# Optimization experiments

Hardware: AMD Instinct MI355X
Metric: run time of the kernel (lower is better)

Reference implementation:

```python
import jax, jax.numpy as jnp
import numpy as np

N = 50000      # nodes
E2 = 400000    # undirected edges
E = 2 * E2     # directed edges (each undirected edge in both directions)
DIN = 512      # input feature dim
DH = 128       # MLP hidden
C = 8          # num classes / BP channels


def setup_inputs() -> dict:
    key = jax.random.key(0)
    ks = jax.random.split(key, 9)
    x = jax.random.normal(ks[0], (N, DIN), jnp.float32)
    src0 = jax.random.randint(ks[1], (E2,), 0, N)
    dst0 = jax.random.randint(ks[2], (E2,), 0, N)
    # symmetric directed edge list: row 0 = source j, row 1 = target i
    edge_index = jnp.stack([jnp.concatenate([src0, dst0]),
                            jnp.concatenate([dst0, src0])])
    w0 = jax.random.uniform(ks[3], (E2,), jnp.float32, 0.5, 1.5)
    edge_weight = jnp.concatenate([w0, w0])  # reverse edge shares weight
    # edge_rv[e] = index of the reverse of edge e
    edge_rv = jnp.concatenate([jnp.arange(E2) + E2, jnp.arange(E2)])
    W1 = jax.random.normal(ks[4], (DIN, DH), jnp.float32) * 0.05
    b1 = jnp.zeros((DH,), jnp.float32)
    W2 = jax.random.normal(ks[5], (DH, C), jnp.float32) * 0.05
    b2 = jnp.zeros((C,), jnp.float32)
    param = jax.random.normal(ks[6], (C, C), jnp.float32) * 0.1
    return {"x": x, "edge_index": edge_index, "edge_weight": edge_weight,
            "edge_rv": edge_rv, "W1": W1, "b1": b1, "W2": W2, "b2": b2,
            "param": param, "K": 5}


def log_normalize(log_x):
    return log_x - jax.nn.logsumexp(log_x, axis=-1, keepdims=True)


def reference(x, edge_index, edge_weight, edge_rv, W1, b1, W2, b2, param, K):
    # MLP transform + LogSoftmax -> initial log-beliefs [N, C]
    h = jax.nn.relu(x @ W1 + b1)
    log_b0 = jax.nn.log_softmax(h @ W2 + b2, axis=-1)

    # learn_H=True: logH = logsigmoid(param + param^T), [C, C]
    logH = jax.nn.log_sigmoid(param + param.T)
    src, dst = edge_index[0], edge_index[1]
    # per-edge coupling matrix [E, C, C]
    logC = edge_weight[:, None, None] * logH[None, :, :]

    log_b = log_b0
    log_msg = None
    for _ in range(K):
        x_j = log_b[src]                       # gather source beliefs [E, C]
        if log_msg is not None:
            x_j = x_j - log_msg[edge_rv]       # remove reverse message
        # tropical-semiring matvec in log domain: logsumexp over source channel
        log_msg = log_normalize(jax.nn.logsumexp(x_j[:, :, None] + logC, axis=1))
        agg = jax.ops.segment_sum(log_msg, dst, num_segments=N)  # scatter-add
        log_b = log_normalize(log_b0 + agg)
    return log_b
```

## Files before the change

kernel.cpp:

```cpp
#include <hip/hip_runtime.h>
#include <hip/hip_bf16.h>
#include <hip/hip_fp16.h>
#include <math.h>

#define NN 50000
#define EE 800000
#define E2K 400000
#define DINK 512
#define DHK 128
#define CK 8
#define KIT 5
#define NBLKS 196
#define NPB 32
#define CAP 1024

typedef __attribute__((ext_vector_type(8))) short short8;
typedef __attribute__((ext_vector_type(4))) float f32x4;

__device__ __forceinline__ unsigned short f2bf(float f) {
    union { float f; unsigned int u; } v;
    v.f = f;
    unsigned int u = v.u;
    unsigned int r = (u + 0x7FFFu + ((u >> 16) & 1u)) >> 16;
    return (unsigned short)r;
}
__device__ __forceinline__ float bfu2f(unsigned int lo16) {
    union { unsigned int u; float f; } v;
    v.u = lo16 << 16;
    return v.f;
}

__global__ __launch_bounds__(256) void prep_kernel(
    const float* __restrict__ W1, const float* __restrict__ param,
    unsigned short* __restrict__ W1t, float* __restrict__ logH) {
    if (blockIdx.x < 256) {
        int idx = blockIdx.x * 256 + threadIdx.x;
        int n = idx >> 9;
        int k = idx & 511;
        W1t[idx] = f2bf(W1[(size_t)k * DHK + n]);
    } else if (threadIdx.x < 64) {
        int t = threadIdx.x;
        int i = t >> 3, j = t & 7;
        float z = param[i * 8 + j] + param[j * 8 + i];
        logH[t] = fminf(z, 0.0f) - log1pf(expf(-fabsf(z)));
    }
}

__global__ __launch_bounds__(256) void mlp_mfma_kernel(
    const float* __restrict__ x, const unsigned short* __restrict__ W1t,
    const float* __restrict__ b1, const float* __restrict__ W2,
    const float* __restrict__ b2, float* __restrict__ logb0) {
    __shared__ unsigned short hs[64 * 136];
    __shared__ float W2s[128 * 8];
    __shared__ float b1s[128];
    __shared__ float b2s[8];

    const int tid = threadIdx.x;
    const int wave = tid >> 6;
    const int lane = tid & 63;
    const int q = lane >> 4;
    const int lm = lane & 15;
    const int wm = wave >> 1, wn = wave & 1;
    const int n0 = blockIdx.x * 64;

    if (tid < 128) b1s[tid] = b1[tid];
    if (tid < 8) b2s[tid] = b2[tid];
    {
        int i = tid * 4;
        *(float4*)&W2s[i] = *(const float4*)&W2[i];
    }
    __syncthreads();

    const float* xptr[2];
#pragma unroll
    for (int mt = 0; mt < 2; ++mt) {
        int r = n0 + wm * 32 + mt * 16 + lm;
        if (r > NN - 1) r = NN - 1;
        xptr[mt] = x + (size_t)r * DINK + q * 8;
    }
    const unsigned short* bptr[4];
#pragma unroll
    for (int nt = 0; nt < 4; ++nt) {
        int c = wn * 64 + nt * 16 + lm;
        bptr[nt] = W1t + (size_t)c * DINK + q * 8;
    }

    f32x4 acc[2][4];
#pragma unroll
    for (int mt = 0; mt < 2; ++mt)
#pragma unroll
        for (int nt = 0; nt < 4; ++nt) acc[mt][nt] = (f32x4){0.f, 0.f, 0.f, 0.f};

    float4 ar[2][2];
    short8 bc[4];
#pragma unroll
    for (int mt = 0; mt < 2; ++mt) {
        ar[mt][0] = *(const float4*)(xptr[mt]);
        ar[mt][1] = *(const float4*)(xptr[mt] + 4);
    }
#pragma unroll
    for (int nt = 0; nt < 4; ++nt) bc[nt] = *(const short8*)(bptr[nt]);

#pragma unroll
    for (int k0 = 32; k0 <= DINK; k0 += 32) {
        float4 ar2[2][2];
        short8 b2f[4];
        if (k0 < DINK) {
#pragma unroll
            for (int mt = 0; mt < 2; ++mt) {
                ar2[mt][0] = *(const float4*)(xptr[mt] + k0);
                ar2[mt][1] = *(const float4*)(xptr[mt] + k0 + 4);
            }
#pragma unroll
            for (int nt = 0; nt < 4; ++nt)
                b2f[nt] = *(const short8*)(bptr[nt] + k0);
        }
        short8 af[2];
#pragma unroll
        for (int mt = 0; mt < 2; ++mt) {
            union { short8 s; __hip_bfloat162 h[4]; } cv;
            cv.h[0] = __float22bfloat162_rn(make_float2(ar[mt][0].x, ar[mt][0].y));
            cv.h[1] = __float22bfloat162_rn(make_float2(ar[mt][0].z, ar[mt][0].w));
            cv.h[2] = __float22bfloat162_rn(make_float2(ar[mt][1].x, ar[mt][1].y));
            cv.h[3] = __float22bfloat162_rn(make_float2(ar[mt][1].z, ar[mt][1].w));
            af[mt] = cv.s;
        }
#pragma unroll
        for (int mt = 0; mt < 2; ++mt)
#pragma unroll
            for (int nt = 0; nt < 4; ++nt)
                acc[mt][nt] = __builtin_amdgcn_mfma_f32_16x16x32_bf16(
                    af[mt], bc[nt], acc[mt][nt], 0, 0, 0);
        if (k0 < DINK) {
#pragma unroll
            for (int mt = 0; mt < 2; ++mt) {
                ar[mt][0] = ar2[mt][0];
                ar[mt][1] = ar2[mt][1];
            }
#pragma unroll
            for (int nt = 0; nt < 4; ++nt) bc[nt] = b2f[nt];
        }
    }

#pragma unroll
    for (int nt = 0; nt < 4; ++nt) {
        int j = wn * 64 + nt * 16 + lm;
        float bj = b1s[j];
#pragma unroll
        for (int mt = 0; mt < 2; ++mt) {
            int rbase = wm * 32 + mt * 16 + q * 4;
#pragma unroll
            for (int r = 0; r < 4; ++r) {
                float h = fmaxf(acc[mt][nt][r] + bj, 0.0f);
                hs[(rbase + r) * 136 + j] = f2bf(h);
            }
        }
    }
    __syncthreads();

    int row = tid >> 2;
    int qh = tid & 3;
    const unsigned short* hp = &hs[row * 136 + qh * 32];
    float p[8] = {0.f, 0.f, 0.f, 0.f, 0.f, 0.f, 0.f, 0.f};
#pragma unroll
    for (int ch = 0; ch < 4; ++ch) {
        uint4 c4 = *(const uint4*)(hp + ch * 8);
        unsigned int uu[4] = {c4.x, c4.y, c4.z, c4.w};
#pragma unroll
        for (int p2 = 0; p2 < 4; ++p2) {
            float h0 = bfu2f(uu[p2] & 0xFFFFu);
            float h1 = bfu2f(uu[p2] >> 16);
            int j = qh * 32 + ch * 8 + p2 * 2;
            const float* w0 = &W2s[j * 8];
            const float* w1 = &W2s[(j + 1) * 8];
#pragma unroll
            for (int c = 0; c < 8; ++c) p[c] = fmaf(h0, w0[c], p[c]);
#pragma unroll
            for (int c = 0; c < 8; ++c) p[c] = fmaf(h1, w1[c], p[c]);
        }
    }
#pragma unroll
    for (int c = 0; c < 8; ++c) p[c] += __shfl_xor(p[c], 1, 64);
#pragma unroll
    for (int c = 0; c < 8; ++c) p[c] += __shfl_xor(p[c], 2, 64);
    int grow = n0 + row;
    if (qh == 0 && grow < NN) {
        float v[8];
        float mx = -1e30f;
#pragma unroll
        for (int c = 0; c < 8; ++c) {
            v[c] = p[c] + b2s[c];
            mx = fmaxf(mx, v[c]);
        }
        float s = 0.0f;
#pragma unroll
        for (int c = 0; c < 8; ++c) s += expf(v[c] - mx);
        float ln = mx + logf(s);
        float4* p0 = (float4*)&logb0[(size_t)grow * 8];
        p0[0] = make_float4(v[0] - ln, v[1] - ln, v[2] - ln, v[3] - ln);
        p0[1] = make_float4(v[4] - ln, v[5] - ln, v[6] - ln, v[7] - ln);
    }
}


__global__ __launch_bounds__(256) void deg_pair_kernel(const int* __restrict__ ei,
                                                       int* __restrict__ cnt) {
    int e = blockIdx.x * 256 + threadIdx.x;
    if (e >= E2K) return;
    int s = ei[e];
    int d = ei[EE + e];
    atomicAdd(&cnt[d], 1);
    atomicAdd(&cnt[s], 1);
}

__global__ __launch_bounds__(256) void scan_partial_kernel(
    const int* __restrict__ cnt, int* __restrict__ partial) {
    __shared__ int sd[256];
    int t = threadIdx.x;
    int i = blockIdx.x * 256 + t;
    sd[t] = (i < NN) ? cnt[i] : 0;
    __syncthreads();
#pragma unroll
    for (int s = 128; s > 0; s >>= 1) {
        if (t < s) sd[t] += sd[t + s];
        __syncthreads();
    }
    if (t == 0) partial[blockIdx.x] = sd[0];
}

__global__ __launch_bounds__(256) void scan_tops_kernel(
    const int* __restrict__ partial, int* __restrict__ tops) {
    __shared__ int sd[256];
    int t = threadIdx.x;
    sd[t] = (t < NBLKS) ? partial[t] : 0;
    __syncthreads();
#pragma unroll
    for (int s = 1; s < 256; s <<= 1) {
        int a = sd[t];
        int b = (t >= s) ? sd[t - s] : 0;
        __syncthreads();
        sd[t] = a + b;
        __syncthreads();
    }
    if (t < NBLKS) tops[t] = (t > 0) ? sd[t - 1] : 0;
}

__global__ __launch_bounds__(256) void scan_write_kernel(
    const int* __restrict__ cnt, const int* __restrict__ tops,
    int* __restrict__ off) {
    __shared__ int sd[256];
    int t = threadIdx.x;
    int i = blockIdx.x * 256 + t;
    int v = (i < NN) ? cnt[i] : 0;
    sd[t] = v;
    __syncthreads();
#pragma unroll
    for (int s = 1; s < 256; s <<= 1) {
        int a = sd[t];
        int b = (t >= s) ? sd[t - s] : 0;
        __syncthreads();
        sd[t] = a + b;
        __syncthreads();
    }
    if (i < NN) off[i] = tops[blockIdx.x] + sd[t] - v;
    if (i == NN - 1) off[NN] = EE;
}

__global__ __launch_bounds__(256) void pos_pair_kernel(
    const int* __restrict__ ei, const float* __restrict__ ew,
    const int* __restrict__ off, int* __restrict__ cnt,
    int2* __restrict__ perm_sw, int2* __restrict__ perm_dr) {
    int e = blockIdx.x * 256 + threadIdx.x;
    if (e >= E2K) return;
    int s = ei[e];
    int d = ei[EE + e];
    int wbits = __float_as_int(ew[e]);
    int pA = off[d] + atomicAdd(&cnt[d], 1);
    int pB = off[s] + atomicAdd(&cnt[s], 1);
    int2 v;
    v.x = s; v.y = wbits; perm_sw[pA] = v;
    v.x = d;              perm_sw[pB] = v;
    v.x = d; v.y = pB;    perm_dr[pA] = v;
    v.x = s; v.y = pA;    perm_dr[pB] = v;
}

__global__ __launch_bounds__(256) void bp_iter_kernel(
    const float* __restrict__ logb0, const int* __restrict__ off,
    const int2* __restrict__ perm_sw, const int2* __restrict__ perm_dr,
    const float* __restrict__ logH, const uint4* __restrict__ msg_prev,
    uint4* __restrict__ msg_next, const float* __restrict__ bel_prev,
    float* __restrict__ bel_next, float* __restrict__ out,
    int first, int last) {
    __shared__ _Float16 smg[CAP * 8];
    __shared__ float lH[64];
    const int t = threadIdx.x;
    if (t < 64) lH[t] = logH[t];

    const int n0 = blockIdx.x * NPB;
    const int nend = (n0 + NPB < NN) ? (n0 + NPB) : NN;
    const int jb0 = off[n0];
    const int jb1 = off[nend];
    const int nl = t >> 3;
    const int c = t & 7;
    const int n = n0 + nl;

    float a = 0.0f;
    int jn0 = 0, jn1 = 0;
    if (n < nend) {
        jn0 = off[n];
        jn1 = off[n + 1];
        a = logb0[(size_t)n * 8 + c];
    }
    __syncthreads();

    for (int cb = jb0; cb < jb1; cb += CAP) {
        int ce = (cb + CAP < jb1) ? (cb + CAP) : jb1;
        for (int j = cb + t; j < ce; j += 256) {
            int2 sw = perm_sw[j];
            float w = __int_as_float(sw.y);
            const float4* pb = (const float4*)&bel_prev[(size_t)sw.x * 8];
            float4 v0 = pb[0], v1 = pb[1];
            float xj[8];
            xj[0] = v0.x; xj[1] = v0.y; xj[2] = v0.z; xj[3] = v0.w;
            xj[4] = v1.x; xj[5] = v1.y; xj[6] = v1.z; xj[7] = v1.w;
            if (!first) {
                int rvp = perm_dr[j].y;
                union { uint4 u; _Float16 h[8]; } mv;
                mv.u = msg_prev[rvp];
#pragma unroll
                for (int k = 0; k < 8; ++k) xj[k] -= (float)mv.h[k];
            }
            float M = xj[0];
#pragma unroll
            for (int k = 1; k < 8; ++k) M = fmaxf(M, xj[k]);
#pragma unroll
            for (int k = 0; k < 8; ++k) xj[k] -= M;
            float mg[8];
#pragma unroll
            for (int c2 = 0; c2 < 8; ++c2) {
                float ssum = 0.0f;
#pragma unroll
                for (int c1 = 0; c1 < 8; ++c1)
                    ssum += __expf(fmaf(w, lH[c1 * 8 + c2], xj[c1]));
                mg[c2] = __logf(ssum);
            }
            float mm = mg[0];
#pragma unroll
            for (int k = 1; k < 8; ++k) mm = fmaxf(mm, mg[k]);
            float se = 0.0f;
#pragma unroll
            for (int k = 0; k < 8; ++k) se += __expf(mg[k] - mm);
            float ln = mm + __logf(se);
            union { uint4 u; _Float16 h[8]; } ov;
#pragma unroll
            for (int k = 0; k < 8; ++k) ov.h[k] = (_Float16)(mg[k] - ln);
            *(uint4*)&smg[(j - cb) * 8] = ov.u;
            if (!last) msg_next[j] = ov.u;
        }
        __syncthreads();
        int lo = (jn0 > cb) ? jn0 : cb;
        int hi = (jn1 < ce) ? jn1 : ce;
        for (int j = lo; j < hi; ++j) a += (float)smg[(j - cb) * 8 + c];
        __syncthreads();
    }

    float mx = a;
#pragma unroll
    for (int s = 1; s < 8; s <<= 1) mx = fmaxf(mx, __shfl_xor(mx, s, 8));
    float sum = __expf(a - mx);
#pragma unroll
    for (int s = 1; s < 8; s <<= 1) sum += __shfl_xor(sum, s, 8);
    float v = a - (mx + __logf(sum));
    if (n < nend) {
        if (last) out[(size_t)n * 8 + c] = v;
        else bel_next[(size_t)n * 8 + c] = v;
    }
}

extern "C" void kernel_launch(void* const* d_in, const int* in_sizes, int n_in,
                              void* d_out, int out_size, void* d_ws, size_t ws_size,
                              hipStream_t stream) {
    const float* x = (const float*)d_in[0];
    const int* ei = (const int*)d_in[1];
    const float* ew = (const float*)d_in[2];
    const float* W1 = (const float*)d_in[4];
    const float* b1 = (const float*)d_in[5];
    const float* W2 = (const float*)d_in[6];
    const float* b2 = (const float*)d_in[7];
    const float* param = (const float*)d_in[8];
    float* out = (float*)d_out;

    float* wsf = (float*)d_ws;
    float* logH = wsf;
    float* logb0 = logH + 64;
    uint4* msgA = (uint4*)(logb0 + (size_t)NN * 8);
    uint4* msgB = msgA + EE;
    int* off = (int*)(msgB + EE);
    int2* perm_sw = (int2*)(off + 50004);
    int2* perm_dr = perm_sw + EE;
    unsigned short* W1t = (unsigned short*)(perm_dr + EE);
    float* belA = (float*)(W1t + 65536);
    float* belB = belA + (size_t)NN * 8;
    int* cnt = (int*)msgA;
    int* partial = cnt + NN;
    int* tops = partial + NBLKS;

    prep_kernel<<<257, 256, 0, stream>>>(W1, param, W1t, logH);
    mlp_mfma_kernel<<<(NN + 63) / 64, 256, 0, stream>>>(x, W1t, b1, W2, b2,
                                                        logb0);

    const int E2B = (E2K + 255) / 256;

    hipMemsetAsync(cnt, 0, (size_t)NN * sizeof(int), stream);
    deg_pair_kernel<<<E2B, 256, 0, stream>>>(ei, cnt);
    scan_partial_kernel<<<NBLKS, 256, 0, stream>>>(cnt, partial);
    scan_tops_kernel<<<1, 256, 0, stream>>>(partial, tops);
    scan_write_kernel<<<NBLKS, 256, 0, stream>>>(cnt, tops, off);
    hipMemsetAsync(cnt, 0, (size_t)NN * sizeof(int), stream);
    pos_pair_kernel<<<E2B, 256, 0, stream>>>(ei, ew, off, cnt, perm_sw, perm_dr);

    const int NB = (NN + NPB - 1) / NPB;
    uint4* msgs[2] = {msgA, msgB};
    float* bels[2] = {belA, belB};
    const float* bprev = logb0;
    for (int it = 0; it < KIT; ++it) {
        bp_iter_kernel<<<NB, 256, 0, stream>>>(
            logb0, off, perm_sw, perm_dr, logH,
            msgs[(it + 1) & 1] , msgs[it & 1] ,
            bprev, bels[it & 1], out,
            it == 0 ? 1 : 0, it == KIT - 1 ? 1 : 0);
        bprev = bels[it & 1];
    }
}
```

Baseline: 466.6 us.

## Split BP iteration into edge-parallel message and node aggregation kernels; enlarge MLP tile

Each fused BP iteration, which computed messages into LDS chunks per 32-node block and then aggregated them, is replaced by two kernels. An edge-parallel msg_kernel handles two edges per thread and always writes messages to global memory. A node-parallel agg_kernel then sums each node's incoming messages from global memory. The reverse-edge table shrinks from int2 to int, which cuts index traffic. The MLP kernel also processes 128 rows per block instead of 64, giving more register accumulators per wave and a 2-way rather than 4-way W2 reduction. In exchange there are extra launches, an added global write and read of messages on the last iteration, and higher register pressure in the MLP kernel.

```diff
diff --git a/kernel.cpp b/kernel.cpp
--- a/kernel.cpp
+++ b/kernel.cpp
@@ -11,8 +11,6 @@
 #define CK 8
 #define KIT 5
 #define NBLKS 196
-#define NPB 32
-#define CAP 1024
 
 typedef __attribute__((ext_vector_type(8))) short short8;
 typedef __attribute__((ext_vector_type(4))) float f32x4;
@@ -50,7 +48,7 @@
     const float* __restrict__ x, const unsigned short* __restrict__ W1t,
     const float* __restrict__ b1, const float* __restrict__ W2,
     const float* __restrict__ b2, float* __restrict__ logb0) {
-    __shared__ unsigned short hs[64 * 136];
+    __shared__ unsigned short hs[128 * 136];
     __shared__ float W2s[128 * 8];
     __shared__ float b1s[128];
     __shared__ float b2s[8];
@@ -61,7 +59,7 @@
     const int q = lane >> 4;
     const int lm = lane & 15;
     const int wm = wave >> 1, wn = wave & 1;
-    const int n0 = blockIdx.x * 64;
+    const int n0 = blockIdx.x * 128;
 
     if (tid < 128) b1s[tid] = b1[tid];
     if (tid < 8) b2s[tid] = b2[tid];
@@ -71,10 +69,10 @@
     }
     __syncthreads();
 
-    const float* xptr[2];
-#pragma unroll
-    for (int mt = 0; mt < 2; ++mt) {
-        int r = n0 + wm * 32 + mt * 16 + lm;
+    const float* xptr[4];
+#pragma unroll
+    for (int mt = 0; mt < 4; ++mt) {
+        int r = n0 + wm * 64 + mt * 16 + lm;
         if (r > NN - 1) r = NN - 1;
         xptr[mt] = x + (size_t)r * DINK + q * 8;
     }
@@ -85,16 +83,16 @@
         bptr[nt] = W1t + (size_t)c * DINK + q * 8;
     }
 
-    f32x4 acc[2][4];
-#pragma unroll
-    for (int mt = 0; mt < 2; ++mt)
+    f32x4 acc[4][4];
+#pragma unroll
+    for (int mt = 0; mt < 4; ++mt)
 #pragma unroll
         for (int nt = 0; nt < 4; ++nt) acc[mt][nt] = (f32x4){0.f, 0.f, 0.f, 0.f};
 
-    float4 ar[2][2];
+    float4 ar[4][2];
     short8 bc[4];
 #pragma unroll
-    for (int mt = 0; mt < 2; ++mt) {
+    for (int mt = 0; mt < 4; ++mt) {
         ar[mt][0] = *(const float4*)(xptr[mt]);
         ar[mt][1] = *(const float4*)(xptr[mt] + 4);
     }
@@ -103,11 +101,11 @@
 
 #pragma unroll
     for (int k0 = 32; k0 <= DINK; k0 += 32) {
-        float4 ar2[2][2];
+        float4 ar2[4][2];
         short8 b2f[4];
         if (k0 < DINK) {
 #pragma unroll
-            for (int mt = 0; mt < 2; ++mt) {
+            for (int mt = 0; mt < 4; ++mt) {
                 ar2[mt][0] = *(const float4*)(xptr[mt] + k0);
                 ar2[mt][1] = *(const float4*)(xptr[mt] + k0 + 4);
             }
@@ -115,9 +113,9 @@
             for (int nt = 0; nt < 4; ++nt)
                 b2f[nt] = *(const short8*)(bptr[nt] + k0);
         }
-        short8 af[2];
-#pragma unroll
-        for (int mt = 0; mt < 2; ++mt) {
+        short8 af[4];
+#pragma unroll
+        for (int mt = 0; mt < 4; ++mt) {
             union { short8 s; __hip_bfloat162 h[4]; } cv;
             cv.h[0] = __float22bfloat162_rn(make_float2(ar[mt][0].x, ar[mt][0].y));
             cv.h[1] = __float22bfloat162_rn(make_float2(ar[mt][0].z, ar[mt][0].w));
@@ -126,14 +124,14 @@
             af[mt] = cv.s;
         }
 #pragma unroll
-        for (int mt = 0; mt < 2; ++mt)
+        for (int mt = 0; mt < 4; ++mt)
 #pragma unroll
             for (int nt = 0; nt < 4; ++nt)
                 acc[mt][nt] = __builtin_amdgcn_mfma_f32_16x16x32_bf16(
                     af[mt], bc[nt], acc[mt][nt], 0, 0, 0);
         if (k0 < DINK) {
 #pragma unroll
-            for (int mt = 0; mt < 2; ++mt) {
+            for (int mt = 0; mt < 4; ++mt) {
                 ar[mt][0] = ar2[mt][0];
                 ar[mt][1] = ar2[mt][1];
             }
@@ -147,8 +145,8 @@
         int j = wn * 64 + nt * 16 + lm;
         float bj = b1s[j];
 #pragma unroll
-        for (int mt = 0; mt < 2; ++mt) {
-            int rbase = wm * 32 + mt * 16 + q * 4;
+        for (int mt = 0; mt < 4; ++mt) {
+            int rbase = wm * 64 + mt * 16 + q * 4;
 #pragma unroll
             for (int r = 0; r < 4; ++r) {
                 float h = fmaxf(acc[mt][nt][r] + bj, 0.0f);
@@ -158,19 +156,19 @@
     }
     __syncthreads();
 
-    int row = tid >> 2;
-    int qh = tid & 3;
-    const unsigned short* hp = &hs[row * 136 + qh * 32];
+    int row = tid >> 1;
+    int half = tid & 1;
+    const unsigned short* hp = &hs[row * 136 + half * 64];
     float p[8] = {0.f, 0.f, 0.f, 0.f, 0.f, 0.f, 0.f, 0.f};
 #pragma unroll
-    for (int ch = 0; ch < 4; ++ch) {
+    for (int ch = 0; ch < 8; ++ch) {
         uint4 c4 = *(const uint4*)(hp + ch * 8);
         unsigned int uu[4] = {c4.x, c4.y, c4.z, c4.w};
 #pragma unroll
         for (int p2 = 0; p2 < 4; ++p2) {
             float h0 = bfu2f(uu[p2] & 0xFFFFu);
             float h1 = bfu2f(uu[p2] >> 16);
-            int j = qh * 32 + ch * 8 + p2 * 2;
+            int j = half * 64 + ch * 8 + p2 * 2;
             const float* w0 = &W2s[j * 8];
             const float* w1 = &W2s[(j + 1) * 8];
 #pragma unroll
@@ -181,10 +179,8 @@
     }
 #pragma unroll
     for (int c = 0; c < 8; ++c) p[c] += __shfl_xor(p[c], 1, 64);
-#pragma unroll
-    for (int c = 0; c < 8; ++c) p[c] += __shfl_xor(p[c], 2, 64);
     int grow = n0 + row;
-    if (qh == 0 && grow < NN) {
+    if (half == 0 && grow < NN) {
         float v[8];
         float mx = -1e30f;
 #pragma unroll
@@ -269,7 +265,7 @@
 __global__ __launch_bounds__(256) void pos_pair_kernel(
     const int* __restrict__ ei, const float* __restrict__ ew,
     const int* __restrict__ off, int* __restrict__ cnt,
-    int2* __restrict__ perm_sw, int2* __restrict__ perm_dr) {
+    int2* __restrict__ perm_sw, int* __restrict__ rvp) {
     int e = blockIdx.x * 256 + threadIdx.x;
     if (e >= E2K) return;
     int s = ei[e];
@@ -280,90 +276,103 @@
     int2 v;
     v.x = s; v.y = wbits; perm_sw[pA] = v;
     v.x = d;              perm_sw[pB] = v;
-    v.x = d; v.y = pB;    perm_dr[pA] = v;
-    v.x = s; v.y = pA;    perm_dr[pB] = v;
-}
-
-__global__ __launch_bounds__(256) void bp_iter_kernel(
-    const float* __restrict__ logb0, const int* __restrict__ off,
-    const int2* __restrict__ perm_sw, const int2* __restrict__ perm_dr,
+    rvp[pA] = pB;
+    rvp[pB] = pA;
+}
+
+__global__ __launch_bounds__(256) void msg_kernel(
+    const int2* __restrict__ perm_sw, const int* __restrict__ rvp,
     const float* __restrict__ logH, const uint4* __restrict__ msg_prev,
-    uint4* __restrict__ msg_next, const float* __restrict__ bel_prev,
-    float* __restrict__ bel_next, float* __restrict__ out,
-    int first, int last) {
-    __shared__ _Float16 smg[CAP * 8];
+    const float* __restrict__ bel_prev, uint4* __restrict__ msg_next,
+    int first) {
     __shared__ float lH[64];
     const int t = threadIdx.x;
     if (t < 64) lH[t] = logH[t];
-
-    const int n0 = blockIdx.x * NPB;
-    const int nend = (n0 + NPB < NN) ? (n0 + NPB) : NN;
-    const int jb0 = off[n0];
-    const int jb1 = off[nend];
-    const int nl = t >> 3;
+    __syncthreads();
+
+    const int base = blockIdx.x * 512 + t;
+    int jj[2];
+    int2 sw[2];
+#pragma unroll
+    for (int e = 0; e < 2; ++e) {
+        int j = base + e * 256;
+        jj[e] = j;
+        int jc = (j < EE) ? j : (EE - 1);
+        sw[e] = perm_sw[jc];
+    }
+    float4 ba[2], bb[2];
+#pragma unroll
+    for (int e = 0; e < 2; ++e) {
+        const float4* pb = (const float4*)&bel_prev[(size_t)sw[e].x * 8];
+        ba[e] = pb[0];
+        bb[e] = pb[1];
+    }
+    uint4 mp[2];
+    if (!first) {
+        int rv[2];
+#pragma unroll
+        for (int e = 0; e < 2; ++e) {
+            int j = jj[e];
+            int jc = (j < EE) ? j : (EE - 1);
+            rv[e] = rvp[jc];
+        }
+#pragma unroll
+        for (int e = 0; e < 2; ++e) mp[e] = msg_prev[rv[e]];
+    }
+
+#pragma unroll
+    for (int e = 0; e < 2; ++e) {
+        float w = __int_as_float(sw[e].y);
+        float xj[8];
+        xj[0] = ba[e].x; xj[1] = ba[e].y; xj[2] = ba[e].z; xj[3] = ba[e].w;
+        xj[4] = bb[e].x; xj[5] = bb[e].y; xj[6] = bb[e].z; xj[7] = bb[e].w;
+        if (!first) {
+            union { uint4 u; _Float16 h[8]; } cv;
+            cv.u = mp[e];
+#pragma unroll
+            for (int k = 0; k < 8; ++k) xj[k] -= (float)cv.h[k];
+        }
+        float M = xj[0];
+#pragma unroll
+        for (int k = 1; k < 8; ++k) M = fmaxf(M, xj[k]);
+#pragma unroll
+        for (int k = 0; k < 8; ++k) xj[k] -= M;
+        float mg[8];
+#pragma unroll
+        for (int c2 = 0; c2 < 8; ++c2) {
+            float ssum = 0.0f;
+#pragma unroll
+            for (int c1 = 0; c1 < 8; ++c1)
+                ssum += __expf(fmaf(w, lH[c1 * 8 + c2], xj[c1]));
+            mg[c2] = __logf(ssum);
+        }
+        float mm = mg[0];
+#pragma unroll
+        for (int k = 1; k < 8; ++k) mm = fmaxf(mm, mg[k]);
+        float se = 0.0f;
+#pragma unroll
+        for (int k = 0; k < 8; ++k) se += __expf(mg[k] - mm);
+        float ln = mm + __logf(se);
+        union { uint4 u; _Float16 h[8]; } ov;
+#pragma unroll
+        for (int k = 0; k < 8; ++k) ov.h[k] = (_Float16)(mg[k] - ln);
+        if (jj[e] < EE) msg_next[jj[e]] = ov.u;
+    }
+}
+
+__global__ __launch_bounds__(256) void agg_kernel(
+    const float* __restrict__ logb0, const int* __restrict__ off,
+    const uint4* __restrict__ msg, float* __restrict__ bel_next,
+    float* __restrict__ out, int last) {
+    const int t = threadIdx.x;
+    const int n = blockIdx.x * 32 + (t >> 3);
     const int c = t & 7;
-    const int n = n0 + nl;
-
-    float a = 0.0f;
-    int jn0 = 0, jn1 = 0;
-    if (n < nend) {
-        jn0 = off[n];
-        jn1 = off[n + 1];
-        a = logb0[(size_t)n * 8 + c];
-    }
-    __syncthreads();
-
-    for (int cb = jb0; cb < jb1; cb += CAP) {
-        int ce = (cb + CAP < jb1) ? (cb + CAP) : jb1;
-        for (int j = cb + t; j < ce; j += 256) {
-            int2 sw = perm_sw[j];
-            float w = __int_as_float(sw.y);
-            const float4* pb = (const float4*)&bel_prev[(size_t)sw.x * 8];
-            float4 v0 = pb[0], v1 = pb[1];
-            float xj[8];
-            xj[0] = v0.x; xj[1] = v0.y; xj[2] = v0.z; xj[3] = v0.w;
-            xj[4] = v1.x; xj[5] = v1.y; xj[6] = v1.z; xj[7] = v1.w;
-            if (!first) {
-                int rvp = perm_dr[j].y;
-                union { uint4 u; _Float16 h[8]; } mv;
-                mv.u = msg_prev[rvp];
-#pragma unroll
-                for (int k = 0; k < 8; ++k) xj[k] -= (float)mv.h[k];
-            }
-            float M = xj[0];
-#pragma unroll
-            for (int k = 1; k < 8; ++k) M = fmaxf(M, xj[k]);
-#pragma unroll
-            for (int k = 0; k < 8; ++k) xj[k] -= M;
-            float mg[8];
-#pragma unroll
-            for (int c2 = 0; c2 < 8; ++c2) {
-                float ssum = 0.0f;
-#pragma unroll
-                for (int c1 = 0; c1 < 8; ++c1)
-                    ssum += __expf(fmaf(w, lH[c1 * 8 + c2], xj[c1]));
-                mg[c2] = __logf(ssum);
-            }
-            float mm = mg[0];
-#pragma unroll
-            for (int k = 1; k < 8; ++k) mm = fmaxf(mm, mg[k]);
-            float se = 0.0f;
-#pragma unroll
-            for (int k = 0; k < 8; ++k) se += __expf(mg[k] - mm);
-            float ln = mm + __logf(se);
-            union { uint4 u; _Float16 h[8]; } ov;
-#pragma unroll
-            for (int k = 0; k < 8; ++k) ov.h[k] = (_Float16)(mg[k] - ln);
-            *(uint4*)&smg[(j - cb) * 8] = ov.u;
-            if (!last) msg_next[j] = ov.u;
-        }
-        __syncthreads();
-        int lo = (jn0 > cb) ? jn0 : cb;
-        int hi = (jn1 < ce) ? jn1 : ce;
-        for (int j = lo; j < hi; ++j) a += (float)smg[(j - cb) * 8 + c];
-        __syncthreads();
-    }
-
+    if (n >= NN) return;
+    float a = logb0[(size_t)n * 8 + c];
+    const int j0 = off[n];
+    const int j1 = off[n + 1];
+    const _Float16* mh = (const _Float16*)msg;
+    for (int j = j0; j < j1; ++j) a += (float)mh[(size_t)j * 8 + c];
     float mx = a;
 #pragma unroll
     for (int s = 1; s < 8; s <<= 1) mx = fmaxf(mx, __shfl_xor(mx, s, 8));
@@ -371,10 +380,8 @@
 #pragma unroll
     for (int s = 1; s < 8; s <<= 1) sum += __shfl_xor(sum, s, 8);
     float v = a - (mx + __logf(sum));
-    if (n < nend) {
-        if (last) out[(size_t)n * 8 + c] = v;
-        else bel_next[(size_t)n * 8 + c] = v;
-    }
+    if (last) out[(size_t)n * 8 + c] = v;
+    else bel_next[(size_t)n * 8 + c] = v;
 }
 
 extern "C" void kernel_launch(void* const* d_in, const int* in_sizes, int n_in,
@@ -397,8 +404,8 @@
     uint4* msgB = msgA + EE;
     int* off = (int*)(msgB + EE);
     int2* perm_sw = (int2*)(off + 50004);
-    int2* perm_dr = perm_sw + EE;
-    unsigned short* W1t = (unsigned short*)(perm_dr + EE);
+    int* rvp = (int*)(perm_sw + EE);
+    unsigned short* W1t = (unsigned short*)(rvp + EE);
     float* belA = (float*)(W1t + 65536);
     float* belB = belA + (size_t)NN * 8;
     int* cnt = (int*)msgA;
@@ -406,8 +413,8 @@
     int* tops = partial + NBLKS;
 
     prep_kernel<<<257, 256, 0, stream>>>(W1, param, W1t, logH);
-    mlp_mfma_kernel<<<(NN + 63) / 64, 256, 0, stream>>>(x, W1t, b1, W2, b2,
-                                                        logb0);
+    mlp_mfma_kernel<<<(NN + 127) / 128, 256, 0, stream>>>(x, W1t, b1, W2, b2,
+                                                          logb0);
 
     const int E2B = (E2K + 255) / 256;
 
@@ -417,18 +424,20 @@
     scan_tops_kernel<<<1, 256, 0, stream>>>(partial, tops);
     scan_write_kernel<<<NBLKS, 256, 0, stream>>>(cnt, tops, off);
     hipMemsetAsync(cnt, 0, (size_t)NN * sizeof(int), stream);
-    pos_pair_kernel<<<E2B, 256, 0, stream>>>(ei, ew, off, cnt, perm_sw, perm_dr);
-
-    const int NB = (NN + NPB - 1) / NPB;
+    pos_pair_kernel<<<E2B, 256, 0, stream>>>(ei, ew, off, cnt, perm_sw, rvp);
+
+    const int MB = (EE + 511) / 512;
+    const int AB = (NN + 31) / 32;
     uint4* msgs[2] = {msgA, msgB};
     float* bels[2] = {belA, belB};
     const float* bprev = logb0;
     for (int it = 0; it < KIT; ++it) {
-        bp_iter_kernel<<<NB, 256, 0, stream>>>(
-            logb0, off, perm_sw, perm_dr, logH,
-            msgs[(it + 1) & 1] , msgs[it & 1] ,
-            bprev, bels[it & 1], out,
-            it == 0 ? 1 : 0, it == KIT - 1 ? 1 : 0);
+        msg_kernel<<<MB, 256, 0, stream>>>(
+            perm_sw, rvp, logH, msgs[(it + 1) & 1] , bprev,
+            msgs[it & 1] , it == 0 ? 1 : 0);
+        agg_kernel<<<AB, 256, 0, stream>>>(
+            logb0, off, msgs[it & 1], bels[it & 1], out,
+            it == KIT - 1 ? 1 : 0);
         bprev = bels[it & 1];
     }
 }
```

Measured after the change: 463.4 us. About the same (-0.7%).
